# Performance work log

Measured on AMD Instinct MI355X. Metric: run time of the kernel, lower is better.

The kernel has to match this reference:

```python
import jax, jax.numpy as jnp
import numpy as np

B, S, D = 8, 2048, 256


def setup_inputs() -> dict:
    key = jax.random.key(0)
    ks = jax.random.split(key, 8)
    nodes = jax.random.normal(ks[0], (B, S, D), dtype=jnp.float32)
    mask = jax.random.randint(ks[1], (B, S), 0, 2, dtype=jnp.int32)
    # ensure at least one unmasked position per row to avoid all--inf softmax
    mask = mask.at[:, 0].set(1)
    scale = 1.0 / np.sqrt(D)
    Wq = jax.random.normal(ks[2], (D, D), dtype=jnp.float32) * scale
    bq = jnp.zeros((D,), dtype=jnp.float32)
    Wk = jax.random.normal(ks[3], (D, D), dtype=jnp.float32) * scale
    bk = jnp.zeros((D,), dtype=jnp.float32)
    Wv = jax.random.normal(ks[4], (D, D), dtype=jnp.float32) * scale
    bv = jnp.zeros((D,), dtype=jnp.float32)
    return {"nodes": nodes, "mask": mask, "Wq": Wq, "bq": bq,
            "Wk": Wk, "bk": bk, "Wv": Wv, "bv": bv}


def reference(nodes, mask, Wq, bq, Wk, bk, Wv, bv):
    # Linear layers: x @ W.T + b (torch nn.Linear convention)
    q = jnp.einsum('bsd,ed->bse', nodes, Wq) + bq   # [B,S,D]
    k = jnp.einsum('bsd,ed->bse', nodes, Wk) + bk
    v = jnp.einsum('bsd,ed->bse', nodes, Wv) + bv
    d = k.shape[-1]
    scores = jnp.einsum('bqd,bkd->bqk', q, k) / jnp.sqrt(jnp.float32(d))  # [B,S,S]
    # mask[b, j] == 0 masks key column j for every query row
    scores = jnp.where(mask[:, None, :] != 0, scores, -jnp.inf)
    attn = jax.nn.softmax(scores, axis=-1)           # [B,S,S]
    weighted = jnp.einsum('bqk,bkd->bqd', attn, v)   # [B,S,D]
    return jnp.mean(weighted, axis=1)                # [B,D]
```

## Files before the change

### kernel.cpp

```cpp
#include <hip/hip_runtime.h>
#include <hip/hip_bf16.h>
#include <stdint.h>


typedef short short8 __attribute__((ext_vector_type(8)));
typedef float floatx4 __attribute__((ext_vector_type(4)));

#define MFMA16(a, b, c) __builtin_amdgcn_mfma_f32_16x16x32_bf16((a), (b), (c), 0, 0, 0)

#define ASYNC16(gsrc, ldst)                                                    \
    __builtin_amdgcn_global_load_lds(                                          \
        (__attribute__((address_space(1))) void*)(void*)(gsrc),                \
        (__attribute__((address_space(3))) void*)(ldst), 16, 0, 0)

static __device__ __forceinline__ unsigned short f2bf(float f) {
    union { float f; unsigned u; } v; v.f = f;
    unsigned r = v.u + 0x7fffu + ((v.u >> 16) & 1u);
    return (unsigned short)(r >> 16);
}
static __device__ __forceinline__ float bf2f(unsigned short h) {
    union { unsigned u; float f; } v; v.u = ((unsigned)h) << 16;
    return v.f;
}

__global__ __launch_bounds__(256) void k_compact2(
    const int* __restrict__ mask, int* __restrict__ cidx, int* __restrict__ cnt,
    float* __restrict__ zbase ,
    float* __restrict__ outp )
{
    int blk = blockIdx.x;
    if (blk < 8) {
        if (threadIdx.x < 64) {
            int b = blk, lane = threadIdx.x;
            int base = 0;
            for (int c = 0; c < 2048; c += 64) {
                int m = mask[b * 2048 + c + lane];
                unsigned long long bal = __ballot(m != 0);
                int pre = __popcll(bal & ((1ull << lane) - 1ull));
                if (m) cidx[b * 2048 + base + pre] = c + lane;
                base += __popcll(bal);
            }
            if (lane == 0) cnt[b] = base;
            for (int i = base + lane; i < 2048; i += 64) cidx[b * 2048 + i] = 0;
        }
        return;
    }
    int idx = (blk - 8) * 256 + threadIdx.x;
    float4 z = {0.f, 0.f, 0.f, 0.f};
#pragma unroll
    for (int j = 0; j < 2; ++j) {
        int p = idx + j * 4352;
        if (p < 8192) ((float4*)zbase)[p] = z;
        else ((float4*)outp)[p - 8192] = z;
    }
}

__global__ __launch_bounds__(256) void k_convert(
    const float* __restrict__ nodes, const float* __restrict__ Wq,
    const float* __restrict__ Wk, const float* __restrict__ Wv,
    unsigned short* __restrict__ nbf, unsigned short* __restrict__ wbf)
{
    int unit = blockIdx.x * 256 + threadIdx.x;
    const float* src;
    unsigned short* dst;
    int off;
    if (unit < 524288) {
        src = nodes; dst = nbf; off = unit * 8;
    } else {
        int j = (unit - 524288) * 8;
        int m = j >> 16;
        int r = j & 65535;
        src = (m == 0) ? Wq : (m == 1 ? Wk : Wv);
        dst = wbf + m * 65536;
        off = r;
    }
    float4 a = *(const float4*)(src + off);
    float4 b = *(const float4*)(src + off + 4);
    short8 o;
    o[0] = f2bf(a.x); o[1] = f2bf(a.y); o[2] = f2bf(a.z); o[3] = f2bf(a.w);
    o[4] = f2bf(b.x); o[5] = f2bf(b.y); o[6] = f2bf(b.z); o[7] = f2bf(b.w);
    *(short8*)(dst + off) = o;
}

__global__ __launch_bounds__(256) void k_proj2a(
    const unsigned short* __restrict__ nbf,
    const unsigned short* __restrict__ wbf,
    const float* __restrict__ bq, const float* __restrict__ bk,
    const float* __restrict__ bv,
    unsigned short* __restrict__ qb, unsigned short* __restrict__ kb,
    unsigned short* __restrict__ vb)
{
    __shared__ __align__(16) unsigned short As[128 * 64];
    __shared__ __align__(16) unsigned short Bs[128 * 64];
    int tid = threadIdx.x, lane = tid & 63, wave = tid >> 6;
    int wm = wave & 1, wn = wave >> 1;
    int l15 = lane & 15, quad = lane >> 4;
    int mBase = blockIdx.x * 128;
    int nBase = blockIdx.y * 128;
    int z = blockIdx.z;
    const unsigned short* W = wbf + z * 65536;

    floatx4 acc[4][4] = {};

    for (int kc = 0; kc < 256; kc += 64) {
#pragma unroll
        for (int i = 0; i < 4; ++i) {
            int p = i * 256 + wave * 64 + lane;
            int row = p >> 3;
            int col8 = (p & 7) ^ (row & 7);
            int goff = row * 256 + kc + col8 * 8;
            unsigned short* dstA = &As[(i * 256 + wave * 64) * 8];
            unsigned short* dstB = &Bs[(i * 256 + wave * 64) * 8];
            ASYNC16(nbf + mBase * 256 + goff, dstA);
            ASYNC16(W + nBase * 256 + goff, dstB);
        }
        __syncthreads();
#pragma unroll
        for (int ks = 0; ks < 2; ++ks) {
            int c8 = ks * 4 + quad;
            short8 af[4], bfr[4];
#pragma unroll
            for (int i = 0; i < 4; ++i) {
                int row = wm * 64 + i * 16 + l15;
                af[i] = *(const short8*)(&As[(row * 8 + (c8 ^ (row & 7))) * 8]);
            }
#pragma unroll
            for (int i = 0; i < 4; ++i) {
                int row = wn * 64 + i * 16 + l15;
                bfr[i] = *(const short8*)(&Bs[(row * 8 + (c8 ^ (row & 7))) * 8]);
            }
#pragma unroll
            for (int mi = 0; mi < 4; ++mi)
#pragma unroll
                for (int ni = 0; ni < 4; ++ni)
                    acc[mi][ni] = MFMA16(af[mi], bfr[ni], acc[mi][ni]);
        }
        __syncthreads();
    }

    const float* bias = (z == 0) ? bq : (z == 1 ? bk : bv);
    unsigned short* out = (z == 0) ? qb : (z == 1 ? kb : vb);
    float scale = (z == 0) ? 0.0625f : 1.0f;
#pragma unroll
    for (int mi = 0; mi < 4; ++mi)
#pragma unroll
        for (int ni = 0; ni < 4; ++ni) {
            int col = nBase + wn * 64 + ni * 16 + l15;
            float bval = bias[col];
#pragma unroll
            for (int r = 0; r < 4; ++r) {
                int row = mBase + wm * 64 + mi * 16 + quad * 4 + r;
                out[row * 256 + col] = f2bf((acc[mi][ni][r] + bval) * scale);
            }
        }
}

__global__ __launch_bounds__(256) void k_repack(
    const unsigned short* __restrict__ kb, const int* __restrict__ cidx,
    const int* __restrict__ cnt_g, unsigned short* __restrict__ kbt)
{
    int c = blockIdx.x, b = blockIdx.y;
    int cnt = cnt_g[b];
    if (c * 64 >= cnt) return;
    size_t obase = ((size_t)b * 32 + c) * 16384;
#pragma unroll
    for (int i = 0; i < 8; ++i) {
        int idx = i * 256 + threadIdx.x;
        int du = idx >> 6, key = idx & 63;
        int krow = cidx[b * 2048 + c * 64 + key];
        short8 v = *(const short8*)(kb + ((size_t)b * 2048 + krow) * 256 + du * 8);
        *(short8*)(kbt + obase + (size_t)idx * 8) = v;
    }
}

__global__ __launch_bounds__(256) void k_pass1t(
    const unsigned short* __restrict__ qb, const unsigned short* __restrict__ kbt,
    const int* __restrict__ cnt_g, float* __restrict__ lsum_g,
    unsigned short* __restrict__ pbuf)
{
    __shared__ __align__(16) unsigned short kt[16384];
    int tid = threadIdx.x, lane = tid & 63, wave = tid >> 6;
    int l15 = lane & 15, quad = lane >> 4;
    int b = blockIdx.z;
    int cnt = cnt_g[b];
    int nchunk = (cnt + 63) >> 6;
    int qBase = blockIdx.x * 128 + wave * 32;
    int qcg = blockIdx.x * 4 + wave;

    short8 qf[2][8];
#pragma unroll
    for (int mi = 0; mi < 2; ++mi)
#pragma unroll
        for (int ks = 0; ks < 8; ++ks)
            qf[mi][ks] = *(const short8*)(qb + (b * 2048 + qBase + mi * 16 + l15) * 256 + ks * 32 + quad * 8);

    float ls[2][4] = {};
    for (int c = blockIdx.y; c < nchunk; c += 4) {
        const unsigned short* src = kbt + ((size_t)b * 32 + c) * 16384;
#pragma unroll
        for (int i = 0; i < 8; ++i) {
            int seg = wave * 8 + i;
            ASYNC16(src + seg * 512 + lane * 8, &kt[seg * 512]);
        }
        __syncthreads();
#pragma unroll
        for (int nt = 0; nt < 4; ++nt) {
            short8 kf[8];
#pragma unroll
            for (int ks = 0; ks < 8; ++ks)
                kf[ks] = *(const short8*)(&kt[((ks * 4 + quad) * 64 + nt * 16 + l15) * 8]);
            floatx4 acc[2] = {};
#pragma unroll
            for (int ks = 0; ks < 8; ++ks) {
                acc[0] = MFMA16(qf[0][ks], kf[ks], acc[0]);
                acc[1] = MFMA16(qf[1][ks], kf[ks], acc[1]);
            }
            float bias = (c * 64 + nt * 16 + l15 < cnt) ? 0.0f : -1e30f;
            short8 hh;
#pragma unroll
            for (int mi = 0; mi < 2; ++mi)
#pragma unroll
                for (int r = 0; r < 4; ++r) {
                    float e = __expf(acc[mi][r] + bias);
                    ls[mi][r] += e;
                    union { _Float16 h; short s; } u; u.h = (_Float16)e;
                    hh[mi * 4 + r] = u.s;
                }
            int ktile = c * 4 + nt;
            if (ktile < 96) {
                size_t off = ((((size_t)b * 96 + ktile) * 64 + qcg) * 64 + lane) * 8;
                *(short8*)(pbuf + off) = hh;
            }
        }
        __syncthreads();
    }
#pragma unroll
    for (int mi = 0; mi < 2; ++mi)
#pragma unroll
        for (int r = 0; r < 4; ++r) {
            float v = ls[mi][r];
            v += __shfl_xor(v, 1); v += __shfl_xor(v, 2);
            v += __shfl_xor(v, 4); v += __shfl_xor(v, 8);
            if (l15 == 0)
                atomicAdd(&lsum_g[b * 2048 + qBase + mi * 16 + quad * 4 + r], v);
        }
}

__global__ __launch_bounds__(512) void k_wred4(
    const unsigned short* __restrict__ pbuf, const float* __restrict__ lsum_g,
    const int* __restrict__ cidx, const int* __restrict__ cnt_g,
    float* __restrict__ wsum_g)
{
    __shared__ float linv_p[2048];
    int tid = threadIdx.x, lane = tid & 63, wave = tid >> 6;
    int l15 = lane & 15, quad = lane >> 4;
    int b = blockIdx.z;
    int ktile = blockIdx.y * 8 + wave;

#pragma unroll
    for (int i = 0; i < 4; ++i) {
        int idx = i * 512 + tid;
        int qcg = idx >> 5, qd = (idx >> 3) & 3, j = idx & 7;
        int q = qcg * 32 + (j >> 2) * 16 + qd * 4 + (j & 3);
        linv_p[idx] = 1.0f / lsum_g[b * 2048 + q];
    }
    __syncthreads();

    int cnt = cnt_g[b];
    if (ktile >= 96 || ktile * 16 >= cnt) return;

    int qcg0 = blockIdx.x * 32;
    float acc = 0.f;
#pragma unroll 4
    for (int qcg = qcg0; qcg < qcg0 + 32; ++qcg) {
        size_t off = ((((size_t)b * 96 + ktile) * 64 + qcg) * 64 + lane) * 8;
        short8 pv = *(const short8*)(pbuf + off);
        const float* lv = &linv_p[(qcg * 4 + quad) * 8];
        floatx4 l0 = *(const floatx4*)lv;
        floatx4 l1 = *(const floatx4*)(lv + 4);
#pragma unroll
        for (int j = 0; j < 4; ++j) {
            union { short s; _Float16 h; } u0, u1;
            u0.s = pv[j]; u1.s = pv[4 + j];
            acc += (float)u0.h * l0[j] + (float)u1.h * l1[j];
        }
    }
    acc += __shfl_xor(acc, 16);
    acc += __shfl_xor(acc, 32);
    int slot = ktile * 16 + l15;
    if (lane < 16 && slot < cnt)
        atomicAdd(&wsum_g[b * 2048 + cidx[b * 2048 + slot]], acc);
}

__global__ __launch_bounds__(256) void k_out(
    const float* __restrict__ wsum_g, const unsigned short* __restrict__ vb,
    float* __restrict__ outp)
{
    int b = blockIdx.y;
    int d = threadIdx.x;
    int k0 = blockIdx.x * 128;
    float acc = 0.f;
#pragma unroll 4
    for (int k = k0; k < k0 + 128; ++k) {
        float wv = wsum_g[b * 2048 + k];
        acc += wv * bf2f(vb[(b * 2048 + k) * 256 + d]);
    }
    atomicAdd(&outp[b * 256 + d], acc * (1.0f / 2048.0f));
}

extern "C" void kernel_launch(void* const* d_in, const int* in_sizes, int n_in,
                              void* d_out, int out_size, void* d_ws, size_t ws_size,
                              hipStream_t stream)
{
    const float* nodes = (const float*)d_in[0];
    const int*   mask  = (const int*)d_in[1];
    const float* Wq    = (const float*)d_in[2];
    const float* bq    = (const float*)d_in[3];
    const float* Wk    = (const float*)d_in[4];
    const float* bk    = (const float*)d_in[5];
    const float* Wv    = (const float*)d_in[6];
    const float* bv    = (const float*)d_in[7];
    float* out = (float*)d_out;

    unsigned short* qb  = (unsigned short*)d_ws;
    unsigned short* kb  = qb + 4194304;
    unsigned short* vb  = kb + 4194304;
    float* lsum = (float*)(vb + 4194304);
    float* wsum = lsum + 16384;
    int*   cnt  = (int*)(wsum + 16384);
    int*   cidx = cnt + 16;
    unsigned short* kbt = (unsigned short*)(cidx + 16384);
    unsigned short* X   = kbt + 4194304;
    unsigned short* nbf = X;
    unsigned short* wbf = X + 4194304;
    unsigned short* pbuf = X;

    k_compact2<<<25, 256, 0, stream>>>(mask, cidx, cnt, lsum, out);
    k_convert<<<2144, 256, 0, stream>>>(nodes, Wq, Wk, Wv, nbf, wbf);
    k_proj2a<<<dim3(128, 2, 3), 256, 0, stream>>>(nbf, wbf, bq, bk, bv, qb, kb, vb);
    k_repack<<<dim3(32, 8), 256, 0, stream>>>(kb, cidx, cnt, kbt);
    k_pass1t<<<dim3(16, 4, 8), 256, 0, stream>>>(qb, kbt, cnt, lsum, pbuf);
    k_wred4<<<dim3(2, 16, 8), 512, 0, stream>>>(pbuf, lsum, cidx, cnt, wsum);
    k_out<<<dim3(16, 8), 256, 0, stream>>>(wsum, vb, out);
}
```

Measured before the change: 146.4 us.

## Store softmax numerators as fp8, widen pass1 query tile, fuse convert with compaction

The unnormalised exp probabilities written to the intermediate buffer are now packed as fp8 instead of fp16, which halves the write traffic in pass1 and the read traffic in the reduction. Pass1 now gives each wave 64 queries instead of 32, so each K tile staged in LDS feeds more MFMAs, and the key-chunk split goes from 4 to 8. The mask compaction and zero-fill are merged into the bf16 conversion launch, saving one kernel launch. The cost is fp8 precision on probabilities, with a risk of accuracy loss or overflow for large exp values, plus higher register pressure from the wider query tile.

```diff
diff --git a/kernel.cpp b/kernel.cpp
--- a/kernel.cpp
+++ b/kernel.cpp
@@ -5,6 +5,7 @@
 
 typedef short short8 __attribute__((ext_vector_type(8)));
 typedef float floatx4 __attribute__((ext_vector_type(4)));
+typedef float floatx2 __attribute__((ext_vector_type(2)));
 
 #define MFMA16(a, b, c) __builtin_amdgcn_mfma_f32_16x16x32_bf16((a), (b), (c), 0, 0, 0)
 
@@ -23,15 +24,41 @@
     return v.f;
 }
 
-__global__ __launch_bounds__(256) void k_compact2(
+__global__ __launch_bounds__(256) void k_cc(
+    const float* __restrict__ nodes, const float* __restrict__ Wq,
+    const float* __restrict__ Wk, const float* __restrict__ Wv,
+    unsigned short* __restrict__ nbf, unsigned short* __restrict__ wbf,
     const int* __restrict__ mask, int* __restrict__ cidx, int* __restrict__ cnt,
     float* __restrict__ zbase ,
     float* __restrict__ outp )
 {
     int blk = blockIdx.x;
-    if (blk < 8) {
+    if (blk < 2144) {
+        int unit = blk * 256 + threadIdx.x;
+        const float* src;
+        unsigned short* dst;
+        int off;
+        if (unit < 524288) {
+            src = nodes; dst = nbf; off = unit * 8;
+        } else {
+            int j = (unit - 524288) * 8;
+            int m = j >> 16;
+            int r = j & 65535;
+            src = (m == 0) ? Wq : (m == 1 ? Wk : Wv);
+            dst = wbf + m * 65536;
+            off = r;
+        }
+        float4 a = *(const float4*)(src + off);
+        float4 b = *(const float4*)(src + off + 4);
+        short8 o;
+        o[0] = f2bf(a.x); o[1] = f2bf(a.y); o[2] = f2bf(a.z); o[3] = f2bf(a.w);
+        o[4] = f2bf(b.x); o[5] = f2bf(b.y); o[6] = f2bf(b.z); o[7] = f2bf(b.w);
+        *(short8*)(dst + off) = o;
+        return;
+    }
+    if (blk < 2152) {
         if (threadIdx.x < 64) {
-            int b = blk, lane = threadIdx.x;
+            int b = blk - 2144, lane = threadIdx.x;
             int base = 0;
             for (int c = 0; c < 2048; c += 64) {
                 int m = mask[b * 2048 + c + lane];
@@ -45,7 +72,7 @@
         }
         return;
     }
-    int idx = (blk - 8) * 256 + threadIdx.x;
+    int idx = (blk - 2152) * 256 + threadIdx.x;
     float4 z = {0.f, 0.f, 0.f, 0.f};
 #pragma unroll
     for (int j = 0; j < 2; ++j) {
@@ -53,33 +80,6 @@
         if (p < 8192) ((float4*)zbase)[p] = z;
         else ((float4*)outp)[p - 8192] = z;
     }
-}
-
-__global__ __launch_bounds__(256) void k_convert(
-    const float* __restrict__ nodes, const float* __restrict__ Wq,
-    const float* __restrict__ Wk, const float* __restrict__ Wv,
-    unsigned short* __restrict__ nbf, unsigned short* __restrict__ wbf)
-{
-    int unit = blockIdx.x * 256 + threadIdx.x;
-    const float* src;
-    unsigned short* dst;
-    int off;
-    if (unit < 524288) {
-        src = nodes; dst = nbf; off = unit * 8;
-    } else {
-        int j = (unit - 524288) * 8;
-        int m = j >> 16;
-        int r = j & 65535;
-        src = (m == 0) ? Wq : (m == 1 ? Wk : Wv);
-        dst = wbf + m * 65536;
-        off = r;
-    }
-    float4 a = *(const float4*)(src + off);
-    float4 b = *(const float4*)(src + off + 4);
-    short8 o;
-    o[0] = f2bf(a.x); o[1] = f2bf(a.y); o[2] = f2bf(a.z); o[3] = f2bf(a.w);
-    o[4] = f2bf(b.x); o[5] = f2bf(b.y); o[6] = f2bf(b.z); o[7] = f2bf(b.w);
-    *(short8*)(dst + off) = o;
 }
 
 __global__ __launch_bounds__(256) void k_proj2a(
@@ -173,10 +173,10 @@
     }
 }
 
-__global__ __launch_bounds__(256) void k_pass1t(
+__global__ __launch_bounds__(256) void k_pass1u(
     const unsigned short* __restrict__ qb, const unsigned short* __restrict__ kbt,
     const int* __restrict__ cnt_g, float* __restrict__ lsum_g,
-    unsigned short* __restrict__ pbuf)
+    unsigned char* __restrict__ pbuf)
 {
     __shared__ __align__(16) unsigned short kt[16384];
     int tid = threadIdx.x, lane = tid & 63, wave = tid >> 6;
@@ -184,18 +184,18 @@
     int b = blockIdx.z;
     int cnt = cnt_g[b];
     int nchunk = (cnt + 63) >> 6;
-    int qBase = blockIdx.x * 128 + wave * 32;
-    int qcg = blockIdx.x * 4 + wave;
-
-    short8 qf[2][8];
-#pragma unroll
-    for (int mi = 0; mi < 2; ++mi)
+    int qBase = blockIdx.x * 256 + wave * 64;
+    int qcg0 = blockIdx.x * 8 + wave * 2;
+
+    short8 qf[4][8];
+#pragma unroll
+    for (int mi = 0; mi < 4; ++mi)
 #pragma unroll
         for (int ks = 0; ks < 8; ++ks)
             qf[mi][ks] = *(const short8*)(qb + (b * 2048 + qBase + mi * 16 + l15) * 256 + ks * 32 + quad * 8);
 
-    float ls[2][4] = {};
-    for (int c = blockIdx.y; c < nchunk; c += 4) {
+    float ls[4][4] = {};
+    for (int c = blockIdx.y; c < nchunk; c += 8) {
         const unsigned short* src = kbt + ((size_t)b * 32 + c) * 16384;
 #pragma unroll
         for (int i = 0; i < 8; ++i) {
@@ -209,33 +209,41 @@
 #pragma unroll
             for (int ks = 0; ks < 8; ++ks)
                 kf[ks] = *(const short8*)(&kt[((ks * 4 + quad) * 64 + nt * 16 + l15) * 8]);
-            floatx4 acc[2] = {};
+            floatx4 acc[4] = {};
 #pragma unroll
             for (int ks = 0; ks < 8; ++ks) {
                 acc[0] = MFMA16(qf[0][ks], kf[ks], acc[0]);
                 acc[1] = MFMA16(qf[1][ks], kf[ks], acc[1]);
+                acc[2] = MFMA16(qf[2][ks], kf[ks], acc[2]);
+                acc[3] = MFMA16(qf[3][ks], kf[ks], acc[3]);
             }
             float bias = (c * 64 + nt * 16 + l15 < cnt) ? 0.0f : -1e30f;
-            short8 hh;
-#pragma unroll
-            for (int mi = 0; mi < 2; ++mi)
+            float e[4][4];
+#pragma unroll
+            for (int mi = 0; mi < 4; ++mi)
 #pragma unroll
                 for (int r = 0; r < 4; ++r) {
-                    float e = __expf(acc[mi][r] + bias);
-                    ls[mi][r] += e;
-                    union { _Float16 h; short s; } u; u.h = (_Float16)e;
-                    hh[mi * 4 + r] = u.s;
+                    e[mi][r] = __expf(acc[mi][r] + bias);
+                    ls[mi][r] += e[mi][r];
                 }
             int ktile = c * 4 + nt;
             if (ktile < 96) {
-                size_t off = ((((size_t)b * 96 + ktile) * 64 + qcg) * 64 + lane) * 8;
-                *(short8*)(pbuf + off) = hh;
+#pragma unroll
+                for (int h = 0; h < 2; ++h) {
+                    int w0 = __builtin_amdgcn_cvt_pk_fp8_f32(e[2*h][0], e[2*h][1], 0, 0);
+                    w0 = __builtin_amdgcn_cvt_pk_fp8_f32(e[2*h][2], e[2*h][3], w0, 1);
+                    int w1 = __builtin_amdgcn_cvt_pk_fp8_f32(e[2*h+1][0], e[2*h+1][1], 0, 0);
+                    w1 = __builtin_amdgcn_cvt_pk_fp8_f32(e[2*h+1][2], e[2*h+1][3], w1, 1);
+                    size_t off = ((((size_t)b * 96 + ktile) * 64 + qcg0 + h) * 64 + lane) * 8;
+                    uint2 pv; pv.x = (unsigned)w0; pv.y = (unsigned)w1;
+                    *(uint2*)(pbuf + off) = pv;
+                }
             }
         }
         __syncthreads();
     }
 #pragma unroll
-    for (int mi = 0; mi < 2; ++mi)
+    for (int mi = 0; mi < 4; ++mi)
 #pragma unroll
         for (int r = 0; r < 4; ++r) {
             float v = ls[mi][r];
@@ -246,8 +254,8 @@
         }
 }
 
-__global__ __launch_bounds__(512) void k_wred4(
-    const unsigned short* __restrict__ pbuf, const float* __restrict__ lsum_g,
+__global__ __launch_bounds__(512) void k_wred5(
+    const unsigned char* __restrict__ pbuf, const float* __restrict__ lsum_g,
     const int* __restrict__ cidx, const int* __restrict__ cnt_g,
     float* __restrict__ wsum_g)
 {
@@ -274,16 +282,14 @@
 #pragma unroll 4
     for (int qcg = qcg0; qcg < qcg0 + 32; ++qcg) {
         size_t off = ((((size_t)b * 96 + ktile) * 64 + qcg) * 64 + lane) * 8;
-        short8 pv = *(const short8*)(pbuf + off);
+        uint2 pv = *(const uint2*)(pbuf + off);
         const float* lv = &linv_p[(qcg * 4 + quad) * 8];
-        floatx4 l0 = *(const floatx4*)lv;
-        floatx4 l1 = *(const floatx4*)(lv + 4);
-#pragma unroll
-        for (int j = 0; j < 4; ++j) {
-            union { short s; _Float16 h; } u0, u1;
-            u0.s = pv[j]; u1.s = pv[4 + j];
-            acc += (float)u0.h * l0[j] + (float)u1.h * l1[j];
-        }
+        floatx2 p01 = __builtin_amdgcn_cvt_pk_f32_fp8(pv.x, 0);
+        floatx2 p23 = __builtin_amdgcn_cvt_pk_f32_fp8(pv.x, 1);
+        floatx2 p45 = __builtin_amdgcn_cvt_pk_f32_fp8(pv.y, 0);
+        floatx2 p67 = __builtin_amdgcn_cvt_pk_f32_fp8(pv.y, 1);
+        acc += p01[0] * lv[0] + p01[1] * lv[1] + p23[0] * lv[2] + p23[1] * lv[3]
+             + p45[0] * lv[4] + p45[1] * lv[5] + p67[0] * lv[6] + p67[1] * lv[7];
     }
     acc += __shfl_xor(acc, 16);
     acc += __shfl_xor(acc, 32);
@@ -333,13 +339,13 @@
     unsigned short* X   = kbt + 4194304;
     unsigned short* nbf = X;
     unsigned short* wbf = X + 4194304;
-    unsigned short* pbuf = X;
-
-    k_compact2<<<25, 256, 0, stream>>>(mask, cidx, cnt, lsum, out);
-    k_convert<<<2144, 256, 0, stream>>>(nodes, Wq, Wk, Wv, nbf, wbf);
+    unsigned char* pbuf = (unsigned char*)X;
+
+    k_cc<<<2169, 256, 0, stream>>>(nodes, Wq, Wk, Wv, nbf, wbf,
+                                   mask, cidx, cnt, lsum, out);
     k_proj2a<<<dim3(128, 2, 3), 256, 0, stream>>>(nbf, wbf, bq, bk, bv, qb, kb, vb);
     k_repack<<<dim3(32, 8), 256, 0, stream>>>(kb, cidx, cnt, kbt);
-    k_pass1t<<<dim3(16, 4, 8), 256, 0, stream>>>(qb, kbt, cnt, lsum, pbuf);
-    k_wred4<<<dim3(2, 16, 8), 512, 0, stream>>>(pbuf, lsum, cidx, cnt, wsum);
+    k_pass1u<<<dim3(8, 8, 8), 256, 0, stream>>>(qb, kbt, cnt, lsum, pbuf);
+    k_wred5<<<dim3(2, 16, 8), 512, 0, stream>>>(pbuf, lsum, cidx, cnt, wsum);
     k_out<<<dim3(16, 8), 256, 0, stream>>>(wsum, vb, out);
 }
```

Result: slower. 152.7 us (+4.4%).
